# Kernel optimization log

Measured on AMD Instinct MI355X. Metric: run time of the kernel, lower is better.

The kernel has to match this reference:

```python
import jax, jax.numpy as jnp
import numpy as np

B, N, QD, OBJ_F, CONV_F = 16384, 6, 11, 10, 100
G_IN = 2 * CONV_F + QD  # 211


def _init_linear(key, fan_in, fan_out):
    kw, kb = jax.random.split(key)
    bound = 1.0 / np.sqrt(fan_in)
    W = jax.random.uniform(kw, (fan_in, fan_out), jnp.float32, -bound, bound)
    b = jax.random.uniform(kb, (fan_out,), jnp.float32, -bound, bound)
    return W, b


def setup_inputs() -> dict:
    key = jax.random.key(0)
    ks = jax.random.split(key, 13)
    tabs = jax.random.normal(ks[0], (B, N, OBJ_F), jnp.float32)
    qst = jax.random.normal(ks[1], (B, QD), jnp.float32)
    Wi1, bi1 = _init_linear(ks[2], 10, 256)
    Wi2, bi2 = _init_linear(ks[3], 256, 128)
    Wi3, bi3 = _init_linear(ks[4], 128, 100)
    Wg1, bg1 = _init_linear(ks[5], G_IN, 256)
    Wg2, bg2 = _init_linear(ks[6], 256, 256)
    Wg3, bg3 = _init_linear(ks[7], 256, 256)
    Wg4, bg4 = _init_linear(ks[8], 256, 256)
    Wf, bf = _init_linear(ks[9], 256, 256)
    Wo1, bo1 = _init_linear(ks[10], 256, 256)
    Wo2, bo2 = _init_linear(ks[11], 256, 10)
    return dict(tabs=tabs, qst=qst, Wi1=Wi1, bi1=bi1, Wi2=Wi2, bi2=bi2,
                Wi3=Wi3, bi3=bi3, Wg1=Wg1, bg1=bg1, Wg2=Wg2, bg2=bg2,
                Wg3=Wg3, bg3=bg3, Wg4=Wg4, bg4=bg4, Wf=Wf, bf=bf,
                Wo1=Wo1, bo1=bo1, Wo2=Wo2, bo2=bo2)


def reference(tabs, qst, Wi1, bi1, Wi2, bi2, Wi3, bi3,
              Wg1, bg1, Wg2, bg2, Wg3, bg3, Wg4, bg4,
              Wf, bf, Wo1, bo1, Wo2, bo2):
    relu = jax.nn.relu
    mb = tabs.shape[0]
    # object encoder: [B, N, 10] -> [B, N, 100]
    x = relu(tabs @ Wi1 + bi1)
    x = relu(x @ Wi2 + bi2)
    x = x @ Wi3 + bi3
    # x_j side carries the question: [B, N, 111]
    xq = jnp.concatenate([x, jnp.broadcast_to(qst[:, None, :], (mb, N, QD))], axis=-1)
    # pairwise features: pair (i, j) = [x[j], x[i], qst]  (matches torch repeat/cat)
    x_i = jnp.broadcast_to(x[:, None, :, :], (mb, N, N, CONV_F))
    x_j = jnp.broadcast_to(xq[:, :, None, :], (mb, N, N, CONV_F + QD))
    pair = jnp.concatenate([x_i, x_j], axis=-1).reshape(mb * N * N, G_IN)
    # g MLP over all pairs
    h = relu(pair @ Wg1 + bg1)
    h = relu(h @ Wg2 + bg2)
    h = relu(h @ Wg3 + bg3)
    h = relu(h @ Wg4 + bg4)
    # sum-pool over the 36 pairs
    g = h.reshape(mb, N * N, 256).sum(axis=1)
    # f MLP + output head (dropout treated as identity / eval mode)
    f = relu(g @ Wf + bf)
    o = relu(f @ Wo1 + bo1)
    logits = o @ Wo2 + bo2
    return jax.nn.log_softmax(logits, axis=1)
```

## Files before the change

### kernel.cpp

```cpp
#include <hip/hip_runtime.h>
#include <hip/hip_bf16.h>
#include <stdint.h>

typedef __attribute__((ext_vector_type(8))) __bf16 bf16x8;
typedef __attribute__((ext_vector_type(8))) short short8v;
typedef __attribute__((ext_vector_type(4))) short short4v;
typedef __attribute__((ext_vector_type(4))) float f32x4;
typedef __attribute__((ext_vector_type(2))) uint32_t u32x2;
typedef __attribute__((ext_vector_type(4))) uint32_t u32x4;

__device__ __forceinline__ float bf2f(short u) {
  return __builtin_bit_cast(float, (uint32_t)((uint32_t)(uint16_t)u << 16));
}
__device__ __forceinline__ short f2bf(float f) {
  uint32_t x = __builtin_bit_cast(uint32_t, f);
  x += 0x7FFFu + ((x >> 16) & 1u);
  return (short)(x >> 16);
}
__device__ __forceinline__ uint32_t cvtpk(float lo, float hi) {
  uint32_t r;
  asm("v_cvt_pk_bf16_f32 %0, %1, %2" : "=v"(r) : "v"(lo), "v"(hi));
  return r;
}
__device__ __forceinline__ f32x4 mfma16(short8v a, short8v b, f32x4 c) {
  return __builtin_amdgcn_mfma_f32_16x16x32_bf16(
      __builtin_bit_cast(bf16x8, a), __builtin_bit_cast(bf16x8, b), c, 0, 0, 0);
}
__device__ __forceinline__ int swz256(int row, int col) {
  return row * 256 + (col ^ ((row & 7) << 3));
}
__device__ __forceinline__ int swz128(int row, int col) {
  return row * 128 + (col ^ ((row & 7) << 3));
}

struct PPDesc { const float* src; short* dst; int Ks, Ns, KT, NT, tile_base; };
struct PPArgs { PPDesc d[11]; int n_desc; int total_tiles; };

__global__ void prepack_all(PPArgs args) {
  int idx = blockIdx.x * 256 + threadIdx.x;
  int tile = idx >> 6;
  if (tile >= args.total_tiles) return;
  int lane = idx & 63;
  int e = 0;
  while (e + 1 < args.n_desc && args.d[e + 1].tile_base <= tile) ++e;
  const PPDesc D = args.d[e];
  int t = tile - D.tile_base;
  int kt = t % D.KT, nt = t / D.KT;
  int n = nt * 16 + (lane & 15);
  int kbase = kt * 32 + ((lane >> 4) * 8);
  short8v o;
#pragma unroll
  for (int j = 0; j < 8; ++j) {
    int k = kbase + j;
    o[j] = f2bf((k < D.Ks && n < D.Ns) ? D.src[k * D.Ns + n] : 0.f);
  }
  *(short8v*)&D.dst[((size_t)t * 64 + lane) * 8] = o;
}

__global__ void qb_kernel(const float* __restrict__ qst, const float* __restrict__ Wg1,
                          const float* __restrict__ bg1, float* __restrict__ qb) {
  int c = threadIdx.x;
  int b0 = blockIdx.x * 32;
  float wcol[11];
#pragma unroll
  for (int k = 0; k < 11; ++k) wcol[k] = Wg1[(200 + k) * 256 + c];
  float bias = bg1[c];
#pragma unroll 1
  for (int bb = 0; bb < 32; ++bb) {
    int b = b0 + bb;
    float acc = bias;
#pragma unroll
    for (int k = 0; k < 11; ++k) acc += qst[b * 11 + k] * wcol[k];
    qb[b * 256 + c] = acc;
  }
}

__launch_bounds__(256, 3)
__global__ void enc_kernel(const float* __restrict__ tabs,
    const float* __restrict__ bi1, const float* __restrict__ bi2, const float* __restrict__ bi3,
    const short* __restrict__ Wi1p, const short* __restrict__ Wi2p, const short* __restrict__ Wi3p,
    const short* __restrict__ Wap, const short* __restrict__ Wbp,
    short* __restrict__ u_g, short* __restrict__ v_g) {
  __shared__ __align__(16) short sIn[64 * 32];
  __shared__ __align__(16) short sH1[64 * 256];
  __shared__ __align__(16) short sH2[64 * 128];
  short* sX = sH1;
  const int tid = threadIdx.x;
  const int lane = tid & 63, w = tid >> 6, quad = lane >> 4, ll = lane & 15;
  const int xl = (ll & 7) << 3;
  const int obj0 = blockIdx.x * 64;

  for (int idx = tid; idx < 64 * 32; idx += 256) {
    int r = idx >> 5, k = idx & 31;
    float v = (k < 10) ? tabs[(obj0 + r) * 10 + k] : 0.f;
    sIn[idx] = f2bf(v);
  }
  __syncthreads();

  {
    f32x4 acc[4][4] = {};
    short8v a[4];
#pragma unroll
    for (int mt = 0; mt < 4; ++mt)
      a[mt] = *(const short8v*)&sIn[(mt * 16 + ll) * 32 + quad * 8];
#pragma unroll
    for (int ni = 0; ni < 4; ++ni) {
      short8v b = *(const short8v*)&Wi1p[((w * 4 + ni) * 64 + lane) * 8];
#pragma unroll
      for (int mt = 0; mt < 4; ++mt) acc[mt][ni] = mfma16(a[mt], b, acc[mt][ni]);
    }
#pragma unroll
    for (int ni = 0; ni < 4; ++ni) {
      int col = (w * 4 + ni) * 16 + ll;
      float bias = bi1[col];
#pragma unroll
      for (int mt = 0; mt < 4; ++mt)
#pragma unroll
        for (int r = 0; r < 4; ++r) {
          int row = mt * 16 + quad * 4 + r;
          sH1[swz256(row, col)] = f2bf(fmaxf(acc[mt][ni][r] + bias, 0.f));
        }
    }
  }
  __syncthreads();

  {
    f32x4 acc[4][2] = {};
#pragma unroll 1
    for (int kt = 0; kt < 8; ++kt) {
      short8v b[2];
#pragma unroll
      for (int ni = 0; ni < 2; ++ni)
        b[ni] = *(const short8v*)&Wi2p[(((w * 2 + ni) * 8 + kt) * 64 + lane) * 8];
#pragma unroll
      for (int mt = 0; mt < 4; ++mt) {
        short8v a = *(const short8v*)&sH1[(mt * 16 + ll) * 256 + ((kt * 32 + quad * 8) ^ xl)];
#pragma unroll
        for (int ni = 0; ni < 2; ++ni) acc[mt][ni] = mfma16(a, b[ni], acc[mt][ni]);
      }
    }
    __syncthreads();
#pragma unroll
    for (int ni = 0; ni < 2; ++ni) {
      int col = (w * 2 + ni) * 16 + ll;
      float bias = bi2[col];
#pragma unroll
      for (int mt = 0; mt < 4; ++mt)
#pragma unroll
        for (int r = 0; r < 4; ++r) {
          int row = mt * 16 + quad * 4 + r;
          sH2[swz128(row, col)] = f2bf(fmaxf(acc[mt][ni][r] + bias, 0.f));
        }
    }
  }
  __syncthreads();

  {
    f32x4 acc[4][2] = {};
#pragma unroll 1
    for (int kt = 0; kt < 4; ++kt) {
      short8v b[2];
#pragma unroll
      for (int ni = 0; ni < 2; ++ni)
        b[ni] = *(const short8v*)&Wi3p[(((w * 2 + ni) * 4 + kt) * 64 + lane) * 8];
#pragma unroll
      for (int mt = 0; mt < 4; ++mt) {
        short8v a = *(const short8v*)&sH2[(mt * 16 + ll) * 128 + ((kt * 32 + quad * 8) ^ xl)];
#pragma unroll
        for (int ni = 0; ni < 2; ++ni) acc[mt][ni] = mfma16(a, b[ni], acc[mt][ni]);
      }
    }
#pragma unroll
    for (int ni = 0; ni < 2; ++ni) {
      int col = (w * 2 + ni) * 16 + ll;
      float bias = (col < 100) ? bi3[col] : 0.f;
#pragma unroll
      for (int mt = 0; mt < 4; ++mt)
#pragma unroll
        for (int r = 0; r < 4; ++r) {
          int row = mt * 16 + quad * 4 + r;
          float vv = (col < 100) ? (acc[mt][ni][r] + bias) : 0.f;
          sX[swz128(row, col)] = f2bf(vv);
        }
    }
  }
  __syncthreads();

#pragma unroll 1
  for (int pass = 0; pass < 2; ++pass) {
    const short* Wp = pass ? Wbp : Wap;
    short* outg = pass ? v_g : u_g;
    f32x4 acc[4][4] = {};
#pragma unroll 1
    for (int kt = 0; kt < 4; ++kt) {
      short8v wv[4];
#pragma unroll
      for (int mi = 0; mi < 4; ++mi)
        wv[mi] = *(const short8v*)&Wp[(((w * 4 + mi) * 4 + kt) * 64 + lane) * 8];
#pragma unroll
      for (int nt = 0; nt < 4; ++nt) {
        short8v xb = *(const short8v*)&sX[(nt * 16 + ll) * 128 + ((kt * 32 + quad * 8) ^ xl)];
#pragma unroll
        for (int mi = 0; mi < 4; ++mi) acc[mi][nt] = mfma16(wv[mi], xb, acc[mi][nt]);
      }
    }
#pragma unroll
    for (int mi = 0; mi < 4; ++mi) {
      int c0 = (w * 4 + mi) * 16 + quad * 4;
#pragma unroll
      for (int nt = 0; nt < 4; ++nt) {
        int obj = obj0 + nt * 16 + ll;
        f32x4 a = acc[mi][nt];
        u32x2 o = {cvtpk(a[0], a[1]), cvtpk(a[2], a[3])};
        *(u32x2*)&outg[(size_t)obj * 256 + c0] = o;
      }
    }
  }
}

__launch_bounds__(512, 4)
__global__ void pair_kernel(const short* __restrict__ u_g, const short* __restrict__ v_g,
    const float* __restrict__ qbp,
    const short* __restrict__ Wg2p, const short* __restrict__ Wg3p, const short* __restrict__ Wg4p,
    const float* __restrict__ bg2, const float* __restrict__ bg3, const float* __restrict__ bg4,
    float* __restrict__ g_g) {
  __shared__ __align__(16) char smem[256 * 104 * 2];
  short* sH = (short*)smem;
  short* sT = (short*)smem;
  const int tid = threadIdx.x;
  const int lane = tid & 63, w = tid >> 6, quad = lane >> 4, ll = lane & 15;
  const int xl = (ll & 7) << 3;
  const int b0 = blockIdx.x * 2;

  if (tid < 256) *(short8v*)&sH[72 * 256 + tid * 8] = short8v{};

#pragma unroll 1
  for (int it = 0; it < 5; ++it) {
    int vi = it * 512 + tid;
    if (vi < 2304) {
      int row = vi >> 5, c8 = (vi & 31) * 8;
      int bb = row / 36, p = row - bb * 36;
      int i2 = p / 6, j2 = p - i2 * 6;
      short8v u8 = *(const short8v*)&u_g[(size_t)((b0 + bb) * 6 + j2) * 256 + c8];
      short8v v8 = *(const short8v*)&v_g[(size_t)((b0 + bb) * 6 + i2) * 256 + c8];
      f32x4 qa = *(const f32x4*)&qbp[(size_t)(b0 + bb) * 256 + c8];
      f32x4 qc = *(const f32x4*)&qbp[(size_t)(b0 + bb) * 256 + c8 + 4];
      float m[8];
#pragma unroll
      for (int e = 0; e < 4; ++e) m[e] = fmaxf(bf2f(u8[e]) + bf2f(v8[e]) + qa[e], 0.f);
#pragma unroll
      for (int e = 0; e < 4; ++e) m[4 + e] = fmaxf(bf2f(u8[4 + e]) + bf2f(v8[4 + e]) + qc[e], 0.f);
      u32x4 o = {cvtpk(m[0], m[1]), cvtpk(m[2], m[3]), cvtpk(m[4], m[5]), cvtpk(m[6], m[7])};
      *(u32x4*)&sH[row * 256 + (c8 ^ ((row & 7) << 3))] = o;
    }
  }
  __syncthreads();

  f32x4 acc[5][2];

#pragma unroll 1
  for (int L = 0; L < 2; ++L) {
    const short* __restrict__ Wp = L ? Wg3p : Wg2p;
    const float* __restrict__ bp = L ? bg3 : bg2;
#pragma unroll
    for (int ni = 0; ni < 2; ++ni) {
      f32x4 b4 = *(const f32x4*)&bp[(w * 2 + ni) * 16 + quad * 4];
#pragma unroll
      for (int mt = 0; mt < 5; ++mt) acc[mt][ni] = b4;
    }
#pragma unroll 1
    for (int kt = 0; kt < 8; ++kt) {
      short8v wv[2];
#pragma unroll
      for (int ni = 0; ni < 2; ++ni)
        wv[ni] = *(const short8v*)&Wp[(((w * 2 + ni) * 8 + kt) * 64 + lane) * 8];
#pragma unroll
      for (int mt = 0; mt < 5; ++mt) {
        short8v h = *(const short8v*)&sH[(mt * 16 + ll) * 256 + ((kt * 32 + quad * 8) ^ xl)];
#pragma unroll
        for (int ni = 0; ni < 2; ++ni) acc[mt][ni] = mfma16(wv[ni], h, acc[mt][ni]);
      }
    }
    __syncthreads();
#pragma unroll
    for (int ni = 0; ni < 2; ++ni) {
      int c0 = (w * 2 + ni) * 16 + quad * 4;
#pragma unroll
      for (int mt = 0; mt < 5; ++mt) {
        int row = mt * 16 + ll;
        f32x4 a = acc[mt][ni];
        u32x2 o = {cvtpk(fmaxf(a[0], 0.f), fmaxf(a[1], 0.f)),
                   cvtpk(fmaxf(a[2], 0.f), fmaxf(a[3], 0.f))};
        *(u32x2*)&sH[row * 256 + (c0 ^ ((row & 7) << 3))] = o;
      }
    }
    __syncthreads();
  }

  {
#pragma unroll
    for (int ni = 0; ni < 2; ++ni) {
      float b = bg4[(w * 2 + ni) * 16 + ll];
#pragma unroll
      for (int mt = 0; mt < 5; ++mt) acc[mt][ni] = f32x4{b, b, b, b};
    }
#pragma unroll 1
    for (int kt = 0; kt < 8; ++kt) {
      short8v bv[2];
#pragma unroll
      for (int ni = 0; ni < 2; ++ni)
        bv[ni] = *(const short8v*)&Wg4p[(((w * 2 + ni) * 8 + kt) * 64 + lane) * 8];
#pragma unroll
      for (int mt = 0; mt < 5; ++mt) {
        short8v a = *(const short8v*)&sH[(mt * 16 + ll) * 256 + ((kt * 32 + quad * 8) ^ xl)];
#pragma unroll
        for (int ni = 0; ni < 2; ++ni) acc[mt][ni] = mfma16(a, bv[ni], acc[mt][ni]);
      }
    }
    __syncthreads();
#pragma unroll
    for (int ni = 0; ni < 2; ++ni) {
      int col = (w * 2 + ni) * 16 + ll;
#pragma unroll
      for (int mt = 0; mt < 5; ++mt) {
        int r0 = mt * 16 + quad * 4;
        f32x4 a = acc[mt][ni];
        u32x2 o = {cvtpk(fmaxf(a[0], 0.f), fmaxf(a[1], 0.f)),
                   cvtpk(fmaxf(a[2], 0.f), fmaxf(a[3], 0.f))};
        *(u32x2*)&sT[col * 104 + r0] = o;
      }
    }
    {
      int col = tid >> 1, seg = tid & 1;
      *(u32x4*)&sT[col * 104 + 80 + seg * 8] = u32x4{0, 0, 0, 0};
    }
    __syncthreads();
  }

  short8v mk[3];
#pragma unroll
  for (int kt = 0; kt < 3; ++kt) {
#pragma unroll
    for (int j = 0; j < 8; ++j) {
      int k = kt * 32 + quad * 8 + j;
      mk[kt][j] = (ll < 2 && (unsigned)(k - ll * 36) < 36u) ? (short)0x3F80 : (short)0;
    }
  }
  f32x4 pa0 = {0.f, 0.f, 0.f, 0.f}, pa1 = {0.f, 0.f, 0.f, 0.f};
#pragma unroll
  for (int kt = 0; kt < 3; ++kt) {
    short8v h0 = *(const short8v*)&sT[((w * 2 + 0) * 16 + ll) * 104 + kt * 32 + quad * 8];
    short8v h1 = *(const short8v*)&sT[((w * 2 + 1) * 16 + ll) * 104 + kt * 32 + quad * 8];
    pa0 = mfma16(mk[kt], h0, pa0);
    pa1 = mfma16(mk[kt], h1, pa1);
  }
  if (quad == 0) {
    int col0 = (w * 2 + 0) * 16 + ll, col1 = (w * 2 + 1) * 16 + ll;
    g_g[(size_t)(b0 + 0) * 256 + col0] = pa0[0];
    g_g[(size_t)(b0 + 1) * 256 + col0] = pa0[1];
    g_g[(size_t)(b0 + 0) * 256 + col1] = pa1[0];
    g_g[(size_t)(b0 + 1) * 256 + col1] = pa1[1];
  }
}

__device__ __forceinline__ void gemm64x256(const short* sInp, short* sOut,
    const short* __restrict__ Wp, const float* __restrict__ bias,
    int w, int lane, int quad, int ll, int xl) {
  f32x4 acc[4][4] = {};
#pragma unroll 1
  for (int kt = 0; kt < 8; ++kt) {
    short8v b[4];
#pragma unroll
    for (int ni = 0; ni < 4; ++ni)
      b[ni] = *(const short8v*)&Wp[(((w * 4 + ni) * 8 + kt) * 64 + lane) * 8];
#pragma unroll
    for (int mt = 0; mt < 4; ++mt) {
      short8v a = *(const short8v*)&sInp[(mt * 16 + ll) * 256 + ((kt * 32 + quad * 8) ^ xl)];
#pragma unroll
      for (int ni = 0; ni < 4; ++ni) acc[mt][ni] = mfma16(a, b[ni], acc[mt][ni]);
    }
  }
#pragma unroll
  for (int ni = 0; ni < 4; ++ni) {
    int col = (w * 4 + ni) * 16 + ll;
    float bv = bias[col];
#pragma unroll
    for (int mt = 0; mt < 4; ++mt)
#pragma unroll
      for (int r = 0; r < 4; ++r) {
        int row = mt * 16 + quad * 4 + r;
        sOut[swz256(row, col)] = f2bf(fmaxf(acc[mt][ni][r] + bv, 0.f));
      }
  }
}

__launch_bounds__(256, 2)
__global__ void head_kernel(const float* __restrict__ g_g,
    const short* __restrict__ Wfp, const float* __restrict__ bf_,
    const short* __restrict__ Wo1p, const float* __restrict__ bo1,
    const short* __restrict__ Wo2p, const float* __restrict__ bo2,
    float* __restrict__ outp) {
  __shared__ __align__(16) short sA[64 * 256];
  __shared__ __align__(16) short sB[64 * 256];
  __shared__ float sL[64 * 16];
  const int tid = threadIdx.x;
  const int lane = tid & 63, w = tid >> 6, quad = lane >> 4, ll = lane & 15;
  const int xl = (ll & 7) << 3;
  const int b0 = blockIdx.x * 64;

#pragma unroll 1
  for (int it = 0; it < 16; ++it) {
    int vi = it * 256 + tid;
    int row = vi >> 6, c4 = (vi & 63) * 4;
    f32x4 gv = *(const f32x4*)&g_g[(b0 + row) * 256 + c4];
    short4v o;
#pragma unroll
    for (int e = 0; e < 4; ++e) o[e] = f2bf(gv[e]);
    *(short4v*)&sA[row * 256 + (c4 ^ ((row & 7) << 3))] = o;
  }
  __syncthreads();
  gemm64x256(sA, sB, Wfp, bf_, w, lane, quad, ll, xl);
  __syncthreads();
  gemm64x256(sB, sA, Wo1p, bo1, w, lane, quad, ll, xl);
  __syncthreads();
  {
    f32x4 acc = {};
#pragma unroll 1
    for (int kt = 0; kt < 8; ++kt) {
      short8v b = *(const short8v*)&Wo2p[(kt * 64 + lane) * 8];
      short8v a = *(const short8v*)&sA[(w * 16 + ll) * 256 + ((kt * 32 + quad * 8) ^ xl)];
      acc = mfma16(a, b, acc);
    }
#pragma unroll
    for (int r = 0; r < 4; ++r) {
      int row = w * 16 + quad * 4 + r;
      sL[row * 16 + ll] = acc[r] + ((ll < 10) ? bo2[ll] : 0.f);
    }
  }
  __syncthreads();
  if (tid < 64) {
    float m = -1e30f;
#pragma unroll
    for (int c = 0; c < 10; ++c) m = fmaxf(m, sL[tid * 16 + c]);
    float s = 0.f;
#pragma unroll
    for (int c = 0; c < 10; ++c) s += expf(sL[tid * 16 + c] - m);
    float ls = logf(s) + m;
#pragma unroll
    for (int c = 0; c < 10; ++c) outp[(b0 + tid) * 10 + c] = sL[tid * 16 + c] - ls;
  }
}

extern "C" void kernel_launch(void* const* d_in, const int* in_sizes, int n_in,
                              void* d_out, int out_size, void* d_ws, size_t ws_size,
                              hipStream_t stream) {
  const float* tabs = (const float*)d_in[0];
  const float* qst  = (const float*)d_in[1];
  const float* Wi1 = (const float*)d_in[2];  const float* bi1 = (const float*)d_in[3];
  const float* Wi2 = (const float*)d_in[4];  const float* bi2 = (const float*)d_in[5];
  const float* Wi3 = (const float*)d_in[6];  const float* bi3 = (const float*)d_in[7];
  const float* Wg1 = (const float*)d_in[8];  const float* bg1 = (const float*)d_in[9];
  const float* Wg2 = (const float*)d_in[10]; const float* bg2 = (const float*)d_in[11];
  const float* Wg3 = (const float*)d_in[12]; const float* bg3 = (const float*)d_in[13];
  const float* Wg4 = (const float*)d_in[14]; const float* bg4 = (const float*)d_in[15];
  const float* Wf  = (const float*)d_in[16]; const float* bf_ = (const float*)d_in[17];
  const float* Wo1 = (const float*)d_in[18]; const float* bo1 = (const float*)d_in[19];
  const float* Wo2 = (const float*)d_in[20]; const float* bo2 = (const float*)d_in[21];
  float* outp = (float*)d_out;
  (void)in_sizes; (void)n_in; (void)out_size; (void)ws_size;

  char* ws = (char*)d_ws;
  size_t off = 0;
  auto alloc = [&](size_t bytes) { void* p = ws + off; off += (bytes + 255) & ~(size_t)255; return p; };
  const size_t BN = 16384ull * 6;
  short* u_g = (short*)alloc(BN * 256 * 2);
  short* v_g = (short*)alloc(BN * 256 * 2);
  float* qb  = (float*)alloc(16384ull * 256 * 4);
  float* g_g = (float*)alloc(16384ull * 256 * 4);
  short* Wi1p = (short*)alloc(16 * 1 * 64 * 8 * 2);
  short* Wi2p = (short*)alloc(8 * 8 * 64 * 8 * 2);
  short* Wi3p = (short*)alloc(8 * 4 * 64 * 8 * 2);
  short* Wap  = (short*)alloc(16 * 4 * 64 * 8 * 2);
  short* Wbp  = (short*)alloc(16 * 4 * 64 * 8 * 2);
  short* Wg2p = (short*)alloc(16 * 8 * 64 * 8 * 2);
  short* Wg3p = (short*)alloc(16 * 8 * 64 * 8 * 2);
  short* Wg4p = (short*)alloc(16 * 8 * 64 * 8 * 2);
  short* Wfp  = (short*)alloc(16 * 8 * 64 * 8 * 2);
  short* Wo1p = (short*)alloc(16 * 8 * 64 * 8 * 2);
  short* Wo2p = (short*)alloc(1 * 8 * 64 * 8 * 2);

  PPArgs pa;
  int tb = 0, nd = 0;
  auto add = [&](const float* src, short* dst, int Ks, int Ns, int KT, int NT) {
    pa.d[nd++] = PPDesc{src, dst, Ks, Ns, KT, NT, tb};
    tb += KT * NT;
  };
  add(Wi1, Wi1p, 10, 256, 1, 16);
  add(Wi2, Wi2p, 256, 128, 8, 8);
  add(Wi3, Wi3p, 128, 100, 4, 8);
  add(Wg1,             Wap, 100, 256, 4, 16);
  add(Wg1 + 100 * 256, Wbp, 100, 256, 4, 16);
  add(Wg2, Wg2p, 256, 256, 8, 16);
  add(Wg3, Wg3p, 256, 256, 8, 16);
  add(Wg4, Wg4p, 256, 256, 8, 16);
  add(Wf,  Wfp,  256, 256, 8, 16);
  add(Wo1, Wo1p, 256, 256, 8, 16);
  add(Wo2, Wo2p, 256, 10, 8, 1);
  pa.n_desc = nd;
  pa.total_tiles = tb;
  prepack_all<<<(tb * 64 + 255) / 256, 256, 0, stream>>>(pa);

  qb_kernel<<<512, 256, 0, stream>>>(qst, Wg1, bg1, qb);
  enc_kernel<<<1536, 256, 0, stream>>>(tabs, bi1, bi2, bi3, Wi1p, Wi2p, Wi3p, Wap, Wbp, u_g, v_g);
  pair_kernel<<<8192, 512, 0, stream>>>(u_g, v_g, qb, Wg2p, Wg3p, Wg4p, bg2, bg3, bg4, g_g);
  head_kernel<<<256, 256, 0, stream>>>(g_g, Wfp, bf_, Wo1p, bo1, Wo2p, bo2, outp);
}
```

Measured before the change: 425.1 us.

## Pool pair outputs in registers, shrink LDS, transpose encoder MFMAs, split head blocks

The pair kernel now sums the final ReLU outputs over the 36 pairs with register adds and cross-lane shuffles, instead of storing a transposed tile to shared memory and reducing it with a mask-matrix MFMA. This frees shared memory, removes two barriers, and allows the occupancy bound to rise from 4 to 8 blocks. The encoder's first two layers are transposed (weights as the A operand) so that bias loads are vectorized and outputs are written as packed bf16. The head kernel processes 32 rows per block over twice as many blocks, which raises parallelism but leaves half the waves idle in the final layer.

```diff
diff --git a/kernel.cpp b/kernel.cpp
--- a/kernel.cpp
+++ b/kernel.cpp
@@ -98,59 +98,71 @@
   __syncthreads();
 
   {
-    f32x4 acc[4][4] = {};
-    short8v a[4];
-#pragma unroll
-    for (int mt = 0; mt < 4; ++mt)
-      a[mt] = *(const short8v*)&sIn[(mt * 16 + ll) * 32 + quad * 8];
-#pragma unroll
-    for (int ni = 0; ni < 4; ++ni) {
-      short8v b = *(const short8v*)&Wi1p[((w * 4 + ni) * 64 + lane) * 8];
-#pragma unroll
-      for (int mt = 0; mt < 4; ++mt) acc[mt][ni] = mfma16(a[mt], b, acc[mt][ni]);
-    }
-#pragma unroll
-    for (int ni = 0; ni < 4; ++ni) {
-      int col = (w * 4 + ni) * 16 + ll;
-      float bias = bi1[col];
-#pragma unroll
-      for (int mt = 0; mt < 4; ++mt)
-#pragma unroll
-        for (int r = 0; r < 4; ++r) {
-          int row = mt * 16 + quad * 4 + r;
-          sH1[swz256(row, col)] = f2bf(fmaxf(acc[mt][ni][r] + bias, 0.f));
-        }
+    f32x4 acc[4][4];
+#pragma unroll
+    for (int mi = 0; mi < 4; ++mi) {
+      f32x4 b4 = *(const f32x4*)&bi1[(w * 4 + mi) * 16 + quad * 4];
+#pragma unroll
+      for (int nt = 0; nt < 4; ++nt) acc[mi][nt] = b4;
+    }
+    short8v wv[4];
+#pragma unroll
+    for (int mi = 0; mi < 4; ++mi)
+      wv[mi] = *(const short8v*)&Wi1p[((w * 4 + mi) * 64 + lane) * 8];
+#pragma unroll
+    for (int nt = 0; nt < 4; ++nt) {
+      short8v a = *(const short8v*)&sIn[(nt * 16 + ll) * 32 + quad * 8];
+#pragma unroll
+      for (int mi = 0; mi < 4; ++mi) acc[mi][nt] = mfma16(wv[mi], a, acc[mi][nt]);
+    }
+#pragma unroll
+    for (int mi = 0; mi < 4; ++mi) {
+      int c0 = (w * 4 + mi) * 16 + quad * 4;
+#pragma unroll
+      for (int nt = 0; nt < 4; ++nt) {
+        int row = nt * 16 + ll;
+        f32x4 a = acc[mi][nt];
+        u32x2 o = {cvtpk(fmaxf(a[0], 0.f), fmaxf(a[1], 0.f)),
+                   cvtpk(fmaxf(a[2], 0.f), fmaxf(a[3], 0.f))};
+        *(u32x2*)&sH1[row * 256 + (c0 ^ ((row & 7) << 3))] = o;
+      }
     }
   }
   __syncthreads();
 
   {
-    f32x4 acc[4][2] = {};
+    f32x4 acc[2][4];
+#pragma unroll
+    for (int mi = 0; mi < 2; ++mi) {
+      f32x4 b4 = *(const f32x4*)&bi2[(w * 2 + mi) * 16 + quad * 4];
+#pragma unroll
+      for (int nt = 0; nt < 4; ++nt) acc[mi][nt] = b4;
+    }
 #pragma unroll 1
     for (int kt = 0; kt < 8; ++kt) {
-      short8v b[2];
-#pragma unroll
-      for (int ni = 0; ni < 2; ++ni)
-        b[ni] = *(const short8v*)&Wi2p[(((w * 2 + ni) * 8 + kt) * 64 + lane) * 8];
-#pragma unroll
-      for (int mt = 0; mt < 4; ++mt) {
-        short8v a = *(const short8v*)&sH1[(mt * 16 + ll) * 256 + ((kt * 32 + quad * 8) ^ xl)];
-#pragma unroll
-        for (int ni = 0; ni < 2; ++ni) acc[mt][ni] = mfma16(a, b[ni], acc[mt][ni]);
+      short8v wv[2];
+#pragma unroll
+      for (int mi = 0; mi < 2; ++mi)
+        wv[mi] = *(const short8v*)&Wi2p[(((w * 2 + mi) * 8 + kt) * 64 + lane) * 8];
+#pragma unroll
+      for (int nt = 0; nt < 4; ++nt) {
+        short8v a = *(const short8v*)&sH1[(nt * 16 + ll) * 256 + ((kt * 32 + quad * 8) ^ xl)];
+#pragma unroll
+        for (int mi = 0; mi < 2; ++mi) acc[mi][nt] = mfma16(wv[mi], a, acc[mi][nt]);
       }
     }
     __syncthreads();
 #pragma unroll
-    for (int ni = 0; ni < 2; ++ni) {
-      int col = (w * 2 + ni) * 16 + ll;
-      float bias = bi2[col];
-#pragma unroll
-      for (int mt = 0; mt < 4; ++mt)
-#pragma unroll
-        for (int r = 0; r < 4; ++r) {
-          int row = mt * 16 + quad * 4 + r;
-          sH2[swz128(row, col)] = f2bf(fmaxf(acc[mt][ni][r] + bias, 0.f));
-        }
+    for (int mi = 0; mi < 2; ++mi) {
+      int c0 = (w * 2 + mi) * 16 + quad * 4;
+#pragma unroll
+      for (int nt = 0; nt < 4; ++nt) {
+        int row = nt * 16 + ll;
+        f32x4 a = acc[mi][nt];
+        u32x2 o = {cvtpk(fmaxf(a[0], 0.f), fmaxf(a[1], 0.f)),
+                   cvtpk(fmaxf(a[2], 0.f), fmaxf(a[3], 0.f))};
+        *(u32x2*)&sH2[row * 128 + (c0 ^ ((row & 7) << 3))] = o;
+      }
     }
   }
   __syncthreads();
@@ -218,15 +230,13 @@
   }
 }
 
-__launch_bounds__(512, 4)
+__launch_bounds__(512, 8)
 __global__ void pair_kernel(const short* __restrict__ u_g, const short* __restrict__ v_g,
     const float* __restrict__ qbp,
     const short* __restrict__ Wg2p, const short* __restrict__ Wg3p, const short* __restrict__ Wg4p,
     const float* __restrict__ bg2, const float* __restrict__ bg3, const float* __restrict__ bg4,
     float* __restrict__ g_g) {
-  __shared__ __align__(16) char smem[256 * 104 * 2];
-  short* sH = (short*)smem;
-  short* sT = (short*)smem;
+  __shared__ __align__(16) short sH[80 * 256];
   const int tid = threadIdx.x;
   const int lane = tid & 63, w = tid >> 6, quad = lane >> 4, ll = lane & 15;
   const int xl = (ll & 7) << 3;
@@ -317,56 +327,34 @@
         for (int ni = 0; ni < 2; ++ni) acc[mt][ni] = mfma16(a, bv[ni], acc[mt][ni]);
       }
     }
-    __syncthreads();
 #pragma unroll
     for (int ni = 0; ni < 2; ++ni) {
       int col = (w * 2 + ni) * 16 + ll;
+      float s0 = 0.f, s1 = 0.f;
 #pragma unroll
       for (int mt = 0; mt < 5; ++mt) {
-        int r0 = mt * 16 + quad * 4;
-        f32x4 a = acc[mt][ni];
-        u32x2 o = {cvtpk(fmaxf(a[0], 0.f), fmaxf(a[1], 0.f)),
-                   cvtpk(fmaxf(a[2], 0.f), fmaxf(a[3], 0.f))};
-        *(u32x2*)&sT[col * 104 + r0] = o;
-      }
-    }
-    {
-      int col = tid >> 1, seg = tid & 1;
-      *(u32x4*)&sT[col * 104 + 80 + seg * 8] = u32x4{0, 0, 0, 0};
-    }
-    __syncthreads();
-  }
-
-  short8v mk[3];
-#pragma unroll
-  for (int kt = 0; kt < 3; ++kt) {
-#pragma unroll
-    for (int j = 0; j < 8; ++j) {
-      int k = kt * 32 + quad * 8 + j;
-      mk[kt][j] = (ll < 2 && (unsigned)(k - ll * 36) < 36u) ? (short)0x3F80 : (short)0;
-    }
-  }
-  f32x4 pa0 = {0.f, 0.f, 0.f, 0.f}, pa1 = {0.f, 0.f, 0.f, 0.f};
-#pragma unroll
-  for (int kt = 0; kt < 3; ++kt) {
-    short8v h0 = *(const short8v*)&sT[((w * 2 + 0) * 16 + ll) * 104 + kt * 32 + quad * 8];
-    short8v h1 = *(const short8v*)&sT[((w * 2 + 1) * 16 + ll) * 104 + kt * 32 + quad * 8];
-    pa0 = mfma16(mk[kt], h0, pa0);
-    pa1 = mfma16(mk[kt], h1, pa1);
-  }
-  if (quad == 0) {
-    int col0 = (w * 2 + 0) * 16 + ll, col1 = (w * 2 + 1) * 16 + ll;
-    g_g[(size_t)(b0 + 0) * 256 + col0] = pa0[0];
-    g_g[(size_t)(b0 + 1) * 256 + col0] = pa0[1];
-    g_g[(size_t)(b0 + 0) * 256 + col1] = pa1[0];
-    g_g[(size_t)(b0 + 1) * 256 + col1] = pa1[1];
-  }
-}
-
-__device__ __forceinline__ void gemm64x256(const short* sInp, short* sOut,
+        int rbase = mt * 16 + quad * 4;
+        float t = 0.f;
+#pragma unroll
+        for (int r = 0; r < 4; ++r) t += fmaxf(acc[mt][ni][r], 0.f);
+        if (rbase < 36) s0 += t;
+        else if (rbase < 72) s1 += t;
+      }
+      s0 += __shfl_xor(s0, 16, 64); s0 += __shfl_xor(s0, 32, 64);
+      s1 += __shfl_xor(s1, 16, 64); s1 += __shfl_xor(s1, 32, 64);
+      if (quad == 0) {
+        g_g[(size_t)(b0 + 0) * 256 + col] = s0;
+        g_g[(size_t)(b0 + 1) * 256 + col] = s1;
+      }
+    }
+  }
+}
+
+template<int MT>
+__device__ __forceinline__ void gemmMx256(const short* sInp, short* sOut,
     const short* __restrict__ Wp, const float* __restrict__ bias,
     int w, int lane, int quad, int ll, int xl) {
-  f32x4 acc[4][4] = {};
+  f32x4 acc[MT][4] = {};
 #pragma unroll 1
   for (int kt = 0; kt < 8; ++kt) {
     short8v b[4];
@@ -374,7 +362,7 @@
     for (int ni = 0; ni < 4; ++ni)
       b[ni] = *(const short8v*)&Wp[(((w * 4 + ni) * 8 + kt) * 64 + lane) * 8];
 #pragma unroll
-    for (int mt = 0; mt < 4; ++mt) {
+    for (int mt = 0; mt < MT; ++mt) {
       short8v a = *(const short8v*)&sInp[(mt * 16 + ll) * 256 + ((kt * 32 + quad * 8) ^ xl)];
 #pragma unroll
       for (int ni = 0; ni < 4; ++ni) acc[mt][ni] = mfma16(a, b[ni], acc[mt][ni]);
@@ -385,7 +373,7 @@
     int col = (w * 4 + ni) * 16 + ll;
     float bv = bias[col];
 #pragma unroll
-    for (int mt = 0; mt < 4; ++mt)
+    for (int mt = 0; mt < MT; ++mt)
 #pragma unroll
       for (int r = 0; r < 4; ++r) {
         int row = mt * 16 + quad * 4 + r;
@@ -394,36 +382,36 @@
   }
 }
 
-__launch_bounds__(256, 2)
+__launch_bounds__(256, 4)
 __global__ void head_kernel(const float* __restrict__ g_g,
     const short* __restrict__ Wfp, const float* __restrict__ bf_,
     const short* __restrict__ Wo1p, const float* __restrict__ bo1,
     const short* __restrict__ Wo2p, const float* __restrict__ bo2,
     float* __restrict__ outp) {
-  __shared__ __align__(16) short sA[64 * 256];
-  __shared__ __align__(16) short sB[64 * 256];
-  __shared__ float sL[64 * 16];
+  __shared__ __align__(16) short sA[32 * 256];
+  __shared__ __align__(16) short sB[32 * 256];
+  __shared__ float sL[32 * 16];
   const int tid = threadIdx.x;
   const int lane = tid & 63, w = tid >> 6, quad = lane >> 4, ll = lane & 15;
   const int xl = (ll & 7) << 3;
-  const int b0 = blockIdx.x * 64;
-
-#pragma unroll 1
-  for (int it = 0; it < 16; ++it) {
+  const int b0 = blockIdx.x * 32;
+
+#pragma unroll 1
+  for (int it = 0; it < 8; ++it) {
     int vi = it * 256 + tid;
     int row = vi >> 6, c4 = (vi & 63) * 4;
-    f32x4 gv = *(const f32x4*)&g_g[(b0 + row) * 256 + c4];
+    f32x4 gv = *(const f32x4*)&g_g[(size_t)(b0 + row) * 256 + c4];
     short4v o;
 #pragma unroll
     for (int e = 0; e < 4; ++e) o[e] = f2bf(gv[e]);
     *(short4v*)&sA[row * 256 + (c4 ^ ((row & 7) << 3))] = o;
   }
   __syncthreads();
-  gemm64x256(sA, sB, Wfp, bf_, w, lane, quad, ll, xl);
-  __syncthreads();
-  gemm64x256(sB, sA, Wo1p, bo1, w, lane, quad, ll, xl);
-  __syncthreads();
-  {
+  gemmMx256<2>(sA, sB, Wfp, bf_, w, lane, quad, ll, xl);
+  __syncthreads();
+  gemmMx256<2>(sB, sA, Wo1p, bo1, w, lane, quad, ll, xl);
+  __syncthreads();
+  if (w < 2) {
     f32x4 acc = {};
 #pragma unroll 1
     for (int kt = 0; kt < 8; ++kt) {
@@ -438,7 +426,7 @@
     }
   }
   __syncthreads();
-  if (tid < 64) {
+  if (tid < 32) {
     float m = -1e30f;
 #pragma unroll
     for (int c = 0; c < 10; ++c) m = fmaxf(m, sL[tid * 16 + c]);
@@ -447,7 +435,7 @@
     for (int c = 0; c < 10; ++c) s += expf(sL[tid * 16 + c] - m);
     float ls = logf(s) + m;
 #pragma unroll
-    for (int c = 0; c < 10; ++c) outp[(b0 + tid) * 10 + c] = sL[tid * 16 + c] - ls;
+    for (int c = 0; c < 10; ++c) outp[(size_t)(b0 + tid) * 10 + c] = sL[tid * 16 + c] - ls;
   }
 }
 
@@ -513,5 +501,5 @@
   qb_kernel<<<512, 256, 0, stream>>>(qst, Wg1, bg1, qb);
   enc_kernel<<<1536, 256, 0, stream>>>(tabs, bi1, bi2, bi3, Wi1p, Wi2p, Wi3p, Wap, Wbp, u_g, v_g);
   pair_kernel<<<8192, 512, 0, stream>>>(u_g, v_g, qb, Wg2p, Wg3p, Wg4p, bg2, bg3, bg4, g_g);
-  head_kernel<<<256, 256, 0, stream>>>(g_g, Wfp, bf_, Wo1p, bo1, Wo2p, bo2, outp);
-}
+  head_kernel<<<512, 256, 0, stream>>>(g_g, Wfp, bf_, Wo1p, bo1, Wo2p, bo2, outp);
+}
```

Result: faster. 411.9 us (-3.1%).
